# Kernel tuning notes

Measured on AMD Instinct MI355X. Metric: run time of the kernel, lower is better.

The kernel has to match this reference:

```python
import jax, jax.numpy as jnp
import numpy as np

DIM = 1024
N_HEADS = 16
HEAD_DIM = DIM // N_HEADS
HIDDEN = 2816
SEQ = 4096
BATCH = 1
NORM_EPS = 1e-5


def setup_inputs() -> dict:
    key = jax.random.key(0)
    ks = jax.random.split(key, 9)
    s = 1.0 / np.sqrt(DIM)
    return {
        "x": jax.random.normal(ks[0], (BATCH, SEQ, DIM), jnp.float32),
        "wq": jax.random.normal(ks[1], (DIM, DIM), jnp.float32) * s,
        "wk": jax.random.normal(ks[2], (DIM, DIM), jnp.float32) * s,
        "wv": jax.random.normal(ks[3], (DIM, DIM), jnp.float32) * s,
        "wo": jax.random.normal(ks[4], (DIM, DIM), jnp.float32) * s,
        "w1": jax.random.normal(ks[5], (DIM, HIDDEN), jnp.float32) * s,
        "w2": jax.random.normal(ks[6], (HIDDEN, DIM), jnp.float32) / np.sqrt(HIDDEN),
        "w3": jax.random.normal(ks[7], (DIM, HIDDEN), jnp.float32) * s,
        "g_attn_norm": jnp.ones((DIM,), jnp.float32),
        "g_ffn_norm": jnp.ones((DIM,), jnp.float32),
    }


def rmsnorm(x, g):
    # x: [b, s, d]; compute in fp32 as in the torch module, then cast back
    xf = x.astype(jnp.float32)
    n = xf * jax.lax.rsqrt(jnp.mean(xf * xf, axis=-1, keepdims=True) + NORM_EPS)
    return n.astype(x.dtype) * g


def attention(x, wq, wk, wv, wo):
    b, s, _ = x.shape
    q = (x @ wq).reshape(b, s, N_HEADS, HEAD_DIM).transpose(0, 2, 1, 3)  # [b,h,s,hd]
    k = (x @ wk).reshape(b, s, N_HEADS, HEAD_DIM).transpose(0, 2, 1, 3)
    v = (x @ wv).reshape(b, s, N_HEADS, HEAD_DIM).transpose(0, 2, 1, 3)
    scores = jnp.einsum("bhqd,bhkd->bhqk", q, k) / np.sqrt(HEAD_DIM)
    causal = jnp.tril(jnp.ones((s, s), bool))
    scores = jnp.where(causal, scores, -jnp.inf)
    probs = jax.nn.softmax(scores.astype(jnp.float32), axis=-1).astype(q.dtype)
    out = jnp.einsum("bhqk,bhkd->bhqd", probs, v)
    out = out.transpose(0, 2, 1, 3).reshape(b, s, DIM)
    return out @ wo


def feed_forward(x, w1, w2, w3):
    return (jax.nn.silu(x @ w1) * (x @ w3)) @ w2


def reference(x, wq, wk, wv, wo, w1, w2, w3, g_attn_norm, g_ffn_norm):
    h = x + attention(rmsnorm(x, g_attn_norm), wq, wk, wv, wo)
    out = h + feed_forward(rmsnorm(h, g_ffn_norm), w1, w2, w3)
    return out
```

## Files before the change

kernel.cpp:

```cpp
#include <hip/hip_runtime.h>
#include <stdint.h>


typedef unsigned short u16;
typedef unsigned int u32;
typedef __attribute__((ext_vector_type(8))) short short8;
typedef __attribute__((ext_vector_type(4))) float f32x4;

#define GLD16(G, L) __builtin_amdgcn_global_load_lds( \
    (__attribute__((address_space(1))) void*)(G),      \
    (__attribute__((address_space(3))) void*)(L), 16, 0, 0)

__device__ __forceinline__ u16 f2bf(float f) {
  u32 u = __builtin_bit_cast(u32, f);
  u32 r = u + 0x7fffu + ((u >> 16) & 1u);
  return (u16)(r >> 16);
}
__device__ __forceinline__ float bf2f(u16 b) {
  u32 u = (u32)b << 16;
  return __builtin_bit_cast(float, u);
}
__device__ __forceinline__ u32 pk_bf16(float lo, float hi) {
  u32 r;
  asm("v_cvt_pk_bf16_f32 %0, %1, %2" : "=v"(r) : "v"(lo), "v"(hi));
  return r;
}

__global__ __launch_bounds__(256) void k_tc4(const float* __restrict__ s0,
                                             const float* __restrict__ s1,
                                             const float* __restrict__ s2,
                                             const float* __restrict__ s3,
                                             u16* __restrict__ out, int R, int C) {
  const int z = blockIdx.z;
  const float* in = (z == 0) ? s0 : (z == 1) ? s1 : (z == 2) ? s2 : s3;
  u16* o = out + (size_t)z * R * C;
  __shared__ float t[32][33];
  const int tx = threadIdx.x & 31, ty = threadIdx.x >> 5;
  const int c0 = blockIdx.x * 32, r0 = blockIdx.y * 32;
#pragma unroll
  for (int i = 0; i < 32; i += 8)
    t[ty + i][tx] = in[(size_t)(r0 + ty + i) * C + (c0 + tx)];
  __syncthreads();
#pragma unroll
  for (int i = 0; i < 32; i += 8)
    o[(size_t)(c0 + ty + i) * R + (r0 + tx)] = f2bf(t[tx][ty + i]);
}

__global__ __launch_bounds__(256) void k_rms(const float* __restrict__ x,
                                             const float* __restrict__ g,
                                             u16* __restrict__ o) {
  const int row = blockIdx.x, tid = threadIdx.x;
  const float4 v = ((const float4*)(x + (size_t)row * 1024))[tid];
  float ss = v.x * v.x + v.y * v.y + v.z * v.z + v.w * v.w;
#pragma unroll
  for (int ofs = 32; ofs > 0; ofs >>= 1) ss += __shfl_xor(ss, ofs);
  __shared__ float red[4];
  if ((tid & 63) == 0) red[tid >> 6] = ss;
  __syncthreads();
  const float s = rsqrtf((red[0] + red[1] + red[2] + red[3]) * (1.f / 1024.f) + 1e-5f);
  const float4 gv = ((const float4*)g)[tid];
  u32 lo = (u32)f2bf(v.x * s * gv.x) | ((u32)f2bf(v.y * s * gv.y) << 16);
  u32 hi = (u32)f2bf(v.z * s * gv.z) | ((u32)f2bf(v.w * s * gv.w) << 16);
  *(uint2*)(o + (size_t)row * 1024 + tid * 4) = make_uint2(lo, hi);
}

template <int EPI, int TN>
__global__ __launch_bounds__(256) void k_gemm(const u16* __restrict__ A,
                                              const u16* __restrict__ Bt,
                                              u16* __restrict__ Obf,
                                              float* __restrict__ Of,
                                              const float* __restrict__ Rz,
                                              int M, int N, int K) {
  constexpr int NFR = TN / 32;
  __shared__ __align__(16) u16 As[2][128 * 32];
  __shared__ __align__(16) u16 Bs[2][TN * 32];
  const int tid = threadIdx.x;
  const int lane = tid & 63, wave = tid >> 6;
  const int wr = wave >> 1, wc = wave & 1;
  const int li = lane & 15, lg = lane >> 4;
  const int row0 = blockIdx.y * 128, col0 = blockIdx.x * TN;

  f32x4 acc[4][NFR] = {};
  const int sr = tid >> 2, sc = (tid & 3) * 8;
  const u16* ag = A + (size_t)(row0 + sr) * K + sc;
  const u16* bg = Bt + (size_t)(col0 + sr) * K + sc;
  const size_t rstep = (size_t)64 * K;

  GLD16(ag, &As[0][tid * 8]);
  GLD16(ag + rstep, &As[0][tid * 8 + 2048]);
  GLD16(bg, &Bs[0][tid * 8]);
  if constexpr (TN == 128) GLD16(bg + rstep, &Bs[0][tid * 8 + 2048]);
  __syncthreads();

  int cur = 0;
  for (int k0 = 0; k0 < K; k0 += 32) {
    const int nxt = cur ^ 1;
    if (k0 + 32 < K) {
      GLD16(ag + k0 + 32, &As[nxt][tid * 8]);
      GLD16(ag + rstep + k0 + 32, &As[nxt][tid * 8 + 2048]);
      GLD16(bg + k0 + 32, &Bs[nxt][tid * 8]);
      if constexpr (TN == 128) GLD16(bg + rstep + k0 + 32, &Bs[nxt][tid * 8 + 2048]);
    }
    short8 af[4], bfr[NFR];
#pragma unroll
    for (int m = 0; m < 4; ++m)
      af[m] = *(const short8*)(&As[cur][(wr * 64 + m * 16 + li) * 32 + lg * 8]);
#pragma unroll
    for (int n = 0; n < NFR; ++n)
      bfr[n] = *(const short8*)(&Bs[cur][(wc * (TN / 2) + n * 16 + li) * 32 + lg * 8]);
#pragma unroll
    for (int m = 0; m < 4; ++m)
#pragma unroll
      for (int n = 0; n < NFR; ++n)
        acc[m][n] = __builtin_amdgcn_mfma_f32_16x16x32_bf16(af[m], bfr[n], acc[m][n], 0, 0, 0);
    __syncthreads();
    cur = nxt;
  }

#pragma unroll
  for (int m = 0; m < 4; ++m) {
    const int row = row0 + wr * 64 + m * 16 + lg * 4;
#pragma unroll
    for (int n = 0; n < NFR; ++n) {
      const int col = col0 + wc * (TN / 2) + n * 16 + li;
#pragma unroll
      for (int r = 0; r < 4; ++r) {
        const size_t idx = (size_t)(row + r) * N + col;
        if (EPI == 0) Obf[idx] = f2bf(acc[m][n][r]);
        else          Of[idx] = acc[m][n][r] + Rz[idx];
      }
    }
  }
}

__global__ __launch_bounds__(256) void k_ffn13(const u16* __restrict__ A,
                                               const u16* __restrict__ B1,
                                               const u16* __restrict__ B3,
                                               u16* __restrict__ O,
                                               int M, int N, int K) {
  __shared__ __align__(16) u16 As[2][128 * 32];
  __shared__ __align__(16) u16 B1s[2][64 * 32];
  __shared__ __align__(16) u16 B3s[2][64 * 32];
  const int tid = threadIdx.x;
  const int lane = tid & 63, wave = tid >> 6;
  const int wr = wave >> 1, wc = wave & 1;
  const int li = lane & 15, lg = lane >> 4;
  const int row0 = blockIdx.y * 128, col0 = blockIdx.x * 64;

  f32x4 a1[4][2] = {}, a3[4][2] = {};
  const int sr = tid >> 2, sc = (tid & 3) * 8;
  const u16* ag = A + (size_t)(row0 + sr) * K + sc;
  const u16* b1g = B1 + (size_t)(col0 + sr) * K + sc;
  const u16* b3g = B3 + (size_t)(col0 + sr) * K + sc;
  const size_t rstep = (size_t)64 * K;

  GLD16(ag, &As[0][tid * 8]);
  GLD16(ag + rstep, &As[0][tid * 8 + 2048]);
  GLD16(b1g, &B1s[0][tid * 8]);
  GLD16(b3g, &B3s[0][tid * 8]);
  __syncthreads();

  int cur = 0;
  for (int k0 = 0; k0 < K; k0 += 32) {
    const int nxt = cur ^ 1;
    if (k0 + 32 < K) {
      GLD16(ag + k0 + 32, &As[nxt][tid * 8]);
      GLD16(ag + rstep + k0 + 32, &As[nxt][tid * 8 + 2048]);
      GLD16(b1g + k0 + 32, &B1s[nxt][tid * 8]);
      GLD16(b3g + k0 + 32, &B3s[nxt][tid * 8]);
    }
    short8 af[4], b1f[2], b3f[2];
#pragma unroll
    for (int m = 0; m < 4; ++m)
      af[m] = *(const short8*)(&As[cur][(wr * 64 + m * 16 + li) * 32 + lg * 8]);
#pragma unroll
    for (int n = 0; n < 2; ++n) {
      b1f[n] = *(const short8*)(&B1s[cur][(wc * 32 + n * 16 + li) * 32 + lg * 8]);
      b3f[n] = *(const short8*)(&B3s[cur][(wc * 32 + n * 16 + li) * 32 + lg * 8]);
    }
#pragma unroll
    for (int m = 0; m < 4; ++m)
#pragma unroll
      for (int n = 0; n < 2; ++n) {
        a1[m][n] = __builtin_amdgcn_mfma_f32_16x16x32_bf16(af[m], b1f[n], a1[m][n], 0, 0, 0);
        a3[m][n] = __builtin_amdgcn_mfma_f32_16x16x32_bf16(af[m], b3f[n], a3[m][n], 0, 0, 0);
      }
    __syncthreads();
    cur = nxt;
  }

#pragma unroll
  for (int m = 0; m < 4; ++m) {
    const int row = row0 + wr * 64 + m * 16 + lg * 4;
#pragma unroll
    for (int n = 0; n < 2; ++n) {
      const int col = col0 + wc * 32 + n * 16 + li;
#pragma unroll
      for (int r = 0; r < 4; ++r) {
        const float g1 = a1[m][n][r], g3 = a3[m][n][r];
        const float sl = g1 / (1.f + __expf(-g1));
        O[(size_t)(row + r) * N + col] = f2bf(sl * g3);
      }
    }
  }
}

__global__ __launch_bounds__(512) void k_attn(const u16* __restrict__ qkv,
                                              u16* __restrict__ Opart,
                                              float* __restrict__ ml) {
  const int LD = 3072;
  const int b = blockIdx.x;
  const int h = b & 15;
  const int p = (b >> 4) >> 1;
  const int j = (b >> 4) & 1;
  const int tid = threadIdx.x, lane = tid & 63, w = tid >> 6;
  const int li = lane & 15, lg = lane >> 4;
  const int swzB = (li & 7) << 4;
  const float QS = 0.125f * 1.44269504f;
  const float FM = 12.0f;

  __shared__ __align__(16) u16 Ks[64 * 64];
  __shared__ __align__(16) u16 Vt[64 * 64];
  __shared__ __align__(16) u16 Ps[8 * 16 * 64];

  const int krow = tid >> 3;
  const u16* kg = qkv + 1024 + h * 64 + ((tid & 7) ^ (krow & 7)) * 8;
  u16* klds = Ks + tid * 8;

  const int vd0 = (tid & 31) * 2;
  const int vkq = tid >> 5;
  const u16* vg = qkv + 2048 + h * 64 + vd0;
  u16* vl0 = Vt + (size_t)vd0 * 64 + (((vkq * 8) ^ ((vd0 & 7) << 4)) >> 1);
  u16* vl1 = Vt + (size_t)(vd0 + 1) * 64 + (((vkq * 8) ^ (((vd0 + 1) & 7) << 4)) >> 1);
  u16* pw = Ps + w * 1024 + li * 64;

  for (int sub = 0; sub < 2; ++sub) {
    const int qb = sub ? (31 - p) : p;
    const int q0 = qb * 128;
    const int t0 = j ? (qb + 1) : 0;
    const int t1 = j ? (2 * qb + 2) : (qb + 1);
    const int qrow = q0 + w * 16 + li;
    const int wqmax = q0 + w * 16 + 15;

    const u16* qp = qkv + (size_t)qrow * LD + h * 64;
    short8 qf0, qf1;
#pragma unroll
    for (int jj = 0; jj < 8; ++jj) {
      qf0[jj] = (short)f2bf(bf2f(qp[lg * 8 + jj]) * QS);
      qf1[jj] = (short)f2bf(bf2f(qp[32 + lg * 8 + jj]) * QS);
    }

    float lsm = 0.f;
    f32x4 accO[4] = {};
    uint4 kld;
    u32 vld[4];
    kld = *(const uint4*)(kg + (size_t)(t0 * 64 + krow) * LD);
#pragma unroll
    for (int i = 0; i < 4; ++i)
      vld[i] = *(const u32*)(vg + (size_t)(t0 * 64 + vkq * 4 + i) * LD);

    for (int t = t0; t < t1; ++t) {
      const int k0 = t * 64;
      __syncthreads();
      *(uint4*)klds = kld;
      {
        u32 lo0 = (vld[0] & 0xffffu) | (vld[1] << 16);
        u32 lo1 = (vld[2] & 0xffffu) | (vld[3] << 16);
        u32 hi0 = (vld[0] >> 16) | (vld[1] & 0xffff0000u);
        u32 hi1 = (vld[2] >> 16) | (vld[3] & 0xffff0000u);
        *(uint2*)vl0 = make_uint2(lo0, lo1);
        *(uint2*)vl1 = make_uint2(hi0, hi1);
      }
      __syncthreads();
      if (t + 1 < t1) {
        kld = *(const uint4*)(kg + (size_t)((t + 1) * 64 + krow) * LD);
        const u16* vp = vg + (size_t)(t + 1) * 64 * LD;
#pragma unroll
        for (int i = 0; i < 4; ++i) vld[i] = *(const u32*)(vp + (size_t)(vkq * 4 + i) * LD);
      }

      if (k0 <= wqmax) {
        f32x4 st[4];
#pragma unroll
        for (int f = 0; f < 4; ++f) {
          const u16* kp = Ks + (size_t)(f * 16 + li) * 64;
          const short8 ka0 = *(const short8*)(kp + (((lg * 16) ^ swzB) >> 1));
          const short8 ka1 = *(const short8*)(kp + (((64 + lg * 16) ^ swzB) >> 1));
          f32x4 z = {-FM, -FM, -FM, -FM};
          z = __builtin_amdgcn_mfma_f32_16x16x32_bf16(ka0, qf0, z, 0, 0, 0);
          st[f] = __builtin_amdgcn_mfma_f32_16x16x32_bf16(ka1, qf1, z, 0, 0, 0);
        }
        if (!(k0 + 63 <= q0 + w * 16)) {
#pragma unroll
          for (int f = 0; f < 4; ++f)
#pragma unroll
            for (int r = 0; r < 4; ++r) {
              const int kg2 = k0 + f * 16 + lg * 4 + r;
              if (kg2 > qrow) st[f][r] = -1e30f;
            }
        }
        float psum = 0.f;
#pragma unroll
        for (int f = 0; f < 4; ++f) {
          const float p0 = __builtin_amdgcn_exp2f(st[f][0]);
          const float p1 = __builtin_amdgcn_exp2f(st[f][1]);
          const float p2 = __builtin_amdgcn_exp2f(st[f][2]);
          const float p3 = __builtin_amdgcn_exp2f(st[f][3]);
          psum += (p0 + p1) + (p2 + p3);
          *(uint2*)(pw + (((f * 32 + lg * 8) ^ swzB) >> 1)) =
              make_uint2(pk_bf16(p0, p1), pk_bf16(p2, p3));
        }
        psum += __shfl_xor(psum, 16);
        psum += __shfl_xor(psum, 32);
        lsm += psum;

#pragma unroll
        for (int kk = 0; kk < 2; ++kk) {
          const int cofs = ((kk * 64 + lg * 16) ^ swzB) >> 1;
          const short8 pf = *(const short8*)(pw + cofs);
#pragma unroll
          for (int n = 0; n < 4; ++n) {
            const short8 vf = *(const short8*)(Vt + (size_t)(n * 16 + li) * 64 + cofs);
            accO[n] = __builtin_amdgcn_mfma_f32_16x16x32_bf16(vf, pf, accO[n], 0, 0, 0);
          }
        }
      }
    }

    const int item = (h * 32 + qb) * 2 + j;
    u16* op = Opart + (size_t)item * 8192 + (w * 16 + li) * 64 + lg * 4;
#pragma unroll
    for (int n = 0; n < 4; ++n)
      *(uint2*)(op + n * 16) = make_uint2(pk_bf16(accO[n][0], accO[n][1]),
                                          pk_bf16(accO[n][2], accO[n][3]));
    if (lg == 0) ml[item * 128 + w * 16 + li] = lsm;
  }
}

__global__ __launch_bounds__(256) void k_amerge(const u16* __restrict__ Opart,
                                                const float* __restrict__ ml,
                                                u16* __restrict__ o) {
  const int b = blockIdx.x;
  const int h = b & 15, qb = b >> 4;
  const int q = threadIdx.x >> 1;
  const int dh = (threadIdx.x & 1) * 32;
  const int i0 = (h * 32 + qb) * 2;
  const float l0 = ml[i0 * 128 + q];
  const float l1 = ml[(i0 + 1) * 128 + q];
  const float r = 1.f / (l0 + l1);
  const u16* p0 = Opart + (size_t)i0 * 8192 + q * 64 + dh;
  const u16* p1 = p0 + 8192;
  u16* op = o + (size_t)(qb * 128 + q) * 1024 + h * 64 + dh;
#pragma unroll
  for (int dd = 0; dd < 32; dd += 4) {
    const uint2 a = *(const uint2*)(p0 + dd);
    const uint2 c = *(const uint2*)(p1 + dd);
    const float s0 = bf2f((u16)a.x) + bf2f((u16)c.x);
    const float s1 = bf2f((u16)(a.x >> 16)) + bf2f((u16)(c.x >> 16));
    const float s2 = bf2f((u16)a.y) + bf2f((u16)c.y);
    const float s3 = bf2f((u16)(a.y >> 16)) + bf2f((u16)(c.y >> 16));
    *(uint2*)(op + dd) = make_uint2(pk_bf16(s0 * r, s1 * r), pk_bf16(s2 * r, s3 * r));
  }
}

extern "C" void kernel_launch(void* const* d_in, const int* in_sizes, int n_in,
                              void* d_out, int out_size, void* d_ws, size_t ws_size,
                              hipStream_t stream) {
  const float* x  = (const float*)d_in[0];
  const float* wq = (const float*)d_in[1];
  const float* wk = (const float*)d_in[2];
  const float* wv = (const float*)d_in[3];
  const float* wo = (const float*)d_in[4];
  const float* w1 = (const float*)d_in[5];
  const float* w2 = (const float*)d_in[6];
  const float* w3 = (const float*)d_in[7];
  const float* ga = (const float*)d_in[8];
  const float* gf = (const float*)d_in[9];
  float* out = (float*)d_out;

  char* p = (char*)d_ws;
  auto take = [&](size_t n) { char* r = p; p += (n + 255) & ~(size_t)255; return r; };
  u16* wqkvo_t = (u16*)take(4ull * 1024 * 1024 * 2);
  u16* w13_t   = (u16*)take(2ull * 2816 * 1024 * 2);
  u16* w2_t    = (u16*)take(1024ull * 2816 * 2);
  u16* xn      = (u16*)take(4096ull * 1024 * 2);
  u16* qkvb    = (u16*)take(4096ull * 3072 * 2);
  u16* atn     = (u16*)take(4096ull * 1024 * 2);
  char* uni    = take(48234496);
  u16* Opart   = (u16*)uni;
  float* mlb   = (float*)(uni + 1024ull * 8192 * 2);
  float* hb    = (float*)uni;
  u16* hn      = (u16*)(uni + 4096ull * 1024 * 4);
  u16* ffb     = (u16*)(uni + 4096ull * 1024 * 6);

  u16* wqkv_t = wqkvo_t;
  u16* wo_t   = wqkvo_t + 3ull * 1024 * 1024;
  u16* w1_t   = w13_t;
  u16* w3_t   = w13_t + 2816ull * 1024;

  k_tc4<<<dim3(32, 32, 4), 256, 0, stream>>>(wq, wk, wv, wo, wqkvo_t, 1024, 1024);
  k_tc4<<<dim3(88, 32, 2), 256, 0, stream>>>(w1, w3, w1, w3, w13_t, 1024, 2816);
  k_tc4<<<dim3(32, 88, 1), 256, 0, stream>>>(w2, w2, w2, w2, w2_t, 2816, 1024);

  k_rms<<<4096, 256, 0, stream>>>(x, ga, xn);
  k_gemm<0, 128><<<dim3(24, 32), 256, 0, stream>>>(xn, wqkv_t, qkvb, nullptr, nullptr, 4096, 3072, 1024);
  k_attn<<<512, 512, 0, stream>>>(qkvb, Opart, mlb);
  k_amerge<<<512, 256, 0, stream>>>(Opart, mlb, atn);
  k_gemm<1, 64><<<dim3(16, 32), 256, 0, stream>>>(atn, wo_t, nullptr, hb, x, 4096, 1024, 1024);
  k_rms<<<4096, 256, 0, stream>>>(hb, gf, hn);
  k_ffn13<<<dim3(44, 32), 256, 0, stream>>>(hn, w1_t, w3_t, ffb, 4096, 2816, 1024);
  k_gemm<1, 64><<<dim3(16, 32), 256, 0, stream>>>(ffb, w2_t, nullptr, out, hb, 4096, 1024, 2816);
}
```

Baseline: 262.3 us.

## Merge weight transpose launches and split attention into one work item per block

The three weight-transpose launches are folded into a single kernel that picks its matrix from a flat block index, which saves two launch overheads. The attention kernel stops pairing a short and a long query block inside one workgroup. It now launches 1024 blocks, each handling one (head, query block, key half) item, with the heaviest query blocks ordered first so the hardware scheduler can balance load dynamically. The cost is more blocks with uneven work, plus repeated per-block setup such as Q fragment loads and pointer math.

```diff
diff --git a/kernel.cpp b/kernel.cpp
--- a/kernel.cpp
+++ b/kernel.cpp
@@ -26,17 +26,41 @@
   return r;
 }
 
-__global__ __launch_bounds__(256) void k_tc4(const float* __restrict__ s0,
-                                             const float* __restrict__ s1,
-                                             const float* __restrict__ s2,
-                                             const float* __restrict__ s3,
-                                             u16* __restrict__ out, int R, int C) {
-  const int z = blockIdx.z;
-  const float* in = (z == 0) ? s0 : (z == 1) ? s1 : (z == 2) ? s2 : s3;
-  u16* o = out + (size_t)z * R * C;
+__global__ __launch_bounds__(256) void k_prep(const float* __restrict__ wq,
+                                              const float* __restrict__ wk,
+                                              const float* __restrict__ wv,
+                                              const float* __restrict__ wo,
+                                              const float* __restrict__ w1,
+                                              const float* __restrict__ w3,
+                                              const float* __restrict__ w2f,
+                                              u16* __restrict__ wqkvo_t,
+                                              u16* __restrict__ w13_t,
+                                              u16* __restrict__ w2_t) {
+  const int bid = blockIdx.x;
+  const float* in;
+  u16* o;
+  int R, C, c0, r0;
+  if (bid < 4096) {
+    const int z = bid >> 10, r = bid & 1023;
+    in = (z == 0) ? wq : (z == 1) ? wk : (z == 2) ? wv : wo;
+    o = wqkvo_t + (size_t)z * 1024 * 1024;
+    R = 1024; C = 1024;
+    c0 = (r & 31) * 32; r0 = (r >> 5) * 32;
+  } else if (bid < 9728) {
+    int r = bid - 4096;
+    const int z = r / 2816; r %= 2816;
+    in = z ? w3 : w1;
+    o = w13_t + (size_t)z * 2816 * 1024;
+    R = 1024; C = 2816;
+    c0 = (r % 88) * 32; r0 = (r / 88) * 32;
+  } else {
+    const int r = bid - 9728;
+    in = w2f; o = w2_t;
+    R = 2816; C = 1024;
+    c0 = (r & 31) * 32; r0 = (r >> 5) * 32;
+  }
   __shared__ float t[32][33];
   const int tx = threadIdx.x & 31, ty = threadIdx.x >> 5;
-  const int c0 = blockIdx.x * 32, r0 = blockIdx.y * 32;
 #pragma unroll
   for (int i = 0; i < 32; i += 8)
     t[ty + i][tx] = in[(size_t)(r0 + ty + i) * C + (c0 + tx)];
@@ -209,10 +233,10 @@
                                               u16* __restrict__ Opart,
                                               float* __restrict__ ml) {
   const int LD = 3072;
-  const int b = blockIdx.x;
-  const int h = b & 15;
-  const int p = (b >> 4) >> 1;
-  const int j = (b >> 4) & 1;
+  const int bid = blockIdx.x;
+  const int qb = 31 - (bid >> 5);
+  const int h = (bid >> 1) & 15;
+  const int j = bid & 1;
   const int tid = threadIdx.x, lane = tid & 63, w = tid >> 6;
   const int li = lane & 15, lg = lane >> 4;
   const int swzB = (li & 7) << 4;
@@ -234,107 +258,104 @@
   u16* vl1 = Vt + (size_t)(vd0 + 1) * 64 + (((vkq * 8) ^ (((vd0 + 1) & 7) << 4)) >> 1);
   u16* pw = Ps + w * 1024 + li * 64;
 
-  for (int sub = 0; sub < 2; ++sub) {
-    const int qb = sub ? (31 - p) : p;
-    const int q0 = qb * 128;
-    const int t0 = j ? (qb + 1) : 0;
-    const int t1 = j ? (2 * qb + 2) : (qb + 1);
-    const int qrow = q0 + w * 16 + li;
-    const int wqmax = q0 + w * 16 + 15;
-
-    const u16* qp = qkv + (size_t)qrow * LD + h * 64;
-    short8 qf0, qf1;
-#pragma unroll
-    for (int jj = 0; jj < 8; ++jj) {
-      qf0[jj] = (short)f2bf(bf2f(qp[lg * 8 + jj]) * QS);
-      qf1[jj] = (short)f2bf(bf2f(qp[32 + lg * 8 + jj]) * QS);
-    }
-
-    float lsm = 0.f;
-    f32x4 accO[4] = {};
-    uint4 kld;
-    u32 vld[4];
-    kld = *(const uint4*)(kg + (size_t)(t0 * 64 + krow) * LD);
-#pragma unroll
-    for (int i = 0; i < 4; ++i)
-      vld[i] = *(const u32*)(vg + (size_t)(t0 * 64 + vkq * 4 + i) * LD);
-
-    for (int t = t0; t < t1; ++t) {
-      const int k0 = t * 64;
-      __syncthreads();
-      *(uint4*)klds = kld;
-      {
-        u32 lo0 = (vld[0] & 0xffffu) | (vld[1] << 16);
-        u32 lo1 = (vld[2] & 0xffffu) | (vld[3] << 16);
-        u32 hi0 = (vld[0] >> 16) | (vld[1] & 0xffff0000u);
-        u32 hi1 = (vld[2] >> 16) | (vld[3] & 0xffff0000u);
-        *(uint2*)vl0 = make_uint2(lo0, lo1);
-        *(uint2*)vl1 = make_uint2(hi0, hi1);
-      }
-      __syncthreads();
-      if (t + 1 < t1) {
-        kld = *(const uint4*)(kg + (size_t)((t + 1) * 64 + krow) * LD);
-        const u16* vp = vg + (size_t)(t + 1) * 64 * LD;
-#pragma unroll
-        for (int i = 0; i < 4; ++i) vld[i] = *(const u32*)(vp + (size_t)(vkq * 4 + i) * LD);
-      }
-
-      if (k0 <= wqmax) {
-        f32x4 st[4];
-#pragma unroll
-        for (int f = 0; f < 4; ++f) {
-          const u16* kp = Ks + (size_t)(f * 16 + li) * 64;
-          const short8 ka0 = *(const short8*)(kp + (((lg * 16) ^ swzB) >> 1));
-          const short8 ka1 = *(const short8*)(kp + (((64 + lg * 16) ^ swzB) >> 1));
-          f32x4 z = {-FM, -FM, -FM, -FM};
-          z = __builtin_amdgcn_mfma_f32_16x16x32_bf16(ka0, qf0, z, 0, 0, 0);
-          st[f] = __builtin_amdgcn_mfma_f32_16x16x32_bf16(ka1, qf1, z, 0, 0, 0);
+  const int q0 = qb * 128;
+  const int t0 = j ? (qb + 1) : 0;
+  const int t1 = j ? (2 * qb + 2) : (qb + 1);
+  const int qrow = q0 + w * 16 + li;
+  const int wqmax = q0 + w * 16 + 15;
+
+  const u16* qp = qkv + (size_t)qrow * LD + h * 64;
+  short8 qf0, qf1;
+#pragma unroll
+  for (int jj = 0; jj < 8; ++jj) {
+    qf0[jj] = (short)f2bf(bf2f(qp[lg * 8 + jj]) * QS);
+    qf1[jj] = (short)f2bf(bf2f(qp[32 + lg * 8 + jj]) * QS);
+  }
+
+  float lsm = 0.f;
+  f32x4 accO[4] = {};
+  uint4 kld;
+  u32 vld[4];
+  kld = *(const uint4*)(kg + (size_t)(t0 * 64 + krow) * LD);
+#pragma unroll
+  for (int i = 0; i < 4; ++i)
+    vld[i] = *(const u32*)(vg + (size_t)(t0 * 64 + vkq * 4 + i) * LD);
+
+  for (int t = t0; t < t1; ++t) {
+    const int k0 = t * 64;
+    __syncthreads();
+    *(uint4*)klds = kld;
+    {
+      u32 lo0 = (vld[0] & 0xffffu) | (vld[1] << 16);
+      u32 lo1 = (vld[2] & 0xffffu) | (vld[3] << 16);
+      u32 hi0 = (vld[0] >> 16) | (vld[1] & 0xffff0000u);
+      u32 hi1 = (vld[2] >> 16) | (vld[3] & 0xffff0000u);
+      *(uint2*)vl0 = make_uint2(lo0, lo1);
+      *(uint2*)vl1 = make_uint2(hi0, hi1);
+    }
+    __syncthreads();
+    if (t + 1 < t1) {
+      kld = *(const uint4*)(kg + (size_t)((t + 1) * 64 + krow) * LD);
+      const u16* vp = vg + (size_t)(t + 1) * 64 * LD;
+#pragma unroll
+      for (int i = 0; i < 4; ++i) vld[i] = *(const u32*)(vp + (size_t)(vkq * 4 + i) * LD);
+    }
+
+    if (k0 <= wqmax) {
+      f32x4 st[4];
+#pragma unroll
+      for (int f = 0; f < 4; ++f) {
+        const u16* kp = Ks + (size_t)(f * 16 + li) * 64;
+        const short8 ka0 = *(const short8*)(kp + (((lg * 16) ^ swzB) >> 1));
+        const short8 ka1 = *(const short8*)(kp + (((64 + lg * 16) ^ swzB) >> 1));
+        f32x4 z = {-FM, -FM, -FM, -FM};
+        z = __builtin_amdgcn_mfma_f32_16x16x32_bf16(ka0, qf0, z, 0, 0, 0);
+        st[f] = __builtin_amdgcn_mfma_f32_16x16x32_bf16(ka1, qf1, z, 0, 0, 0);
+      }
+      if (!(k0 + 63 <= q0 + w * 16)) {
+#pragma unroll
+        for (int f = 0; f < 4; ++f)
+#pragma unroll
+          for (int r = 0; r < 4; ++r) {
+            const int kg2 = k0 + f * 16 + lg * 4 + r;
+            if (kg2 > qrow) st[f][r] = -1e30f;
+          }
+      }
+      float psum = 0.f;
+#pragma unroll
+      for (int f = 0; f < 4; ++f) {
+        const float p0 = __builtin_amdgcn_exp2f(st[f][0]);
+        const float p1 = __builtin_amdgcn_exp2f(st[f][1]);
+        const float p2 = __builtin_amdgcn_exp2f(st[f][2]);
+        const float p3 = __builtin_amdgcn_exp2f(st[f][3]);
+        psum += (p0 + p1) + (p2 + p3);
+        *(uint2*)(pw + (((f * 32 + lg * 8) ^ swzB) >> 1)) =
+            make_uint2(pk_bf16(p0, p1), pk_bf16(p2, p3));
+      }
+      psum += __shfl_xor(psum, 16);
+      psum += __shfl_xor(psum, 32);
+      lsm += psum;
+
+#pragma unroll
+      for (int kk = 0; kk < 2; ++kk) {
+        const int cofs = ((kk * 64 + lg * 16) ^ swzB) >> 1;
+        const short8 pf = *(const short8*)(pw + cofs);
+#pragma unroll
+        for (int n = 0; n < 4; ++n) {
+          const short8 vf = *(const short8*)(Vt + (size_t)(n * 16 + li) * 64 + cofs);
+          accO[n] = __builtin_amdgcn_mfma_f32_16x16x32_bf16(vf, pf, accO[n], 0, 0, 0);
         }
-        if (!(k0 + 63 <= q0 + w * 16)) {
-#pragma unroll
-          for (int f = 0; f < 4; ++f)
-#pragma unroll
-            for (int r = 0; r < 4; ++r) {
-              const int kg2 = k0 + f * 16 + lg * 4 + r;
-              if (kg2 > qrow) st[f][r] = -1e30f;
-            }
-        }
-        float psum = 0.f;
-#pragma unroll
-        for (int f = 0; f < 4; ++f) {
-          const float p0 = __builtin_amdgcn_exp2f(st[f][0]);
-          const float p1 = __builtin_amdgcn_exp2f(st[f][1]);
-          const float p2 = __builtin_amdgcn_exp2f(st[f][2]);
-          const float p3 = __builtin_amdgcn_exp2f(st[f][3]);
-          psum += (p0 + p1) + (p2 + p3);
-          *(uint2*)(pw + (((f * 32 + lg * 8) ^ swzB) >> 1)) =
-              make_uint2(pk_bf16(p0, p1), pk_bf16(p2, p3));
-        }
-        psum += __shfl_xor(psum, 16);
-        psum += __shfl_xor(psum, 32);
-        lsm += psum;
-
-#pragma unroll
-        for (int kk = 0; kk < 2; ++kk) {
-          const int cofs = ((kk * 64 + lg * 16) ^ swzB) >> 1;
-          const short8 pf = *(const short8*)(pw + cofs);
-#pragma unroll
-          for (int n = 0; n < 4; ++n) {
-            const short8 vf = *(const short8*)(Vt + (size_t)(n * 16 + li) * 64 + cofs);
-            accO[n] = __builtin_amdgcn_mfma_f32_16x16x32_bf16(vf, pf, accO[n], 0, 0, 0);
-          }
-        }
-      }
-    }
-
-    const int item = (h * 32 + qb) * 2 + j;
-    u16* op = Opart + (size_t)item * 8192 + (w * 16 + li) * 64 + lg * 4;
-#pragma unroll
-    for (int n = 0; n < 4; ++n)
-      *(uint2*)(op + n * 16) = make_uint2(pk_bf16(accO[n][0], accO[n][1]),
-                                          pk_bf16(accO[n][2], accO[n][3]));
-    if (lg == 0) ml[item * 128 + w * 16 + li] = lsm;
-  }
+      }
+    }
+  }
+
+  const int item = (h * 32 + qb) * 2 + j;
+  u16* op = Opart + (size_t)item * 8192 + (w * 16 + li) * 64 + lg * 4;
+#pragma unroll
+  for (int n = 0; n < 4; ++n)
+    *(uint2*)(op + n * 16) = make_uint2(pk_bf16(accO[n][0], accO[n][1]),
+                                        pk_bf16(accO[n][2], accO[n][3]));
+  if (lg == 0) ml[item * 128 + w * 16 + li] = lsm;
 }
 
 __global__ __launch_bounds__(256) void k_amerge(const u16* __restrict__ Opart,
@@ -398,13 +419,11 @@
   u16* w1_t   = w13_t;
   u16* w3_t   = w13_t + 2816ull * 1024;
 
-  k_tc4<<<dim3(32, 32, 4), 256, 0, stream>>>(wq, wk, wv, wo, wqkvo_t, 1024, 1024);
-  k_tc4<<<dim3(88, 32, 2), 256, 0, stream>>>(w1, w3, w1, w3, w13_t, 1024, 2816);
-  k_tc4<<<dim3(32, 88, 1), 256, 0, stream>>>(w2, w2, w2, w2, w2_t, 2816, 1024);
+  k_prep<<<12544, 256, 0, stream>>>(wq, wk, wv, wo, w1, w3, w2, wqkvo_t, w13_t, w2_t);
 
   k_rms<<<4096, 256, 0, stream>>>(x, ga, xn);
   k_gemm<0, 128><<<dim3(24, 32), 256, 0, stream>>>(xn, wqkv_t, qkvb, nullptr, nullptr, 4096, 3072, 1024);
-  k_attn<<<512, 512, 0, stream>>>(qkvb, Opart, mlb);
+  k_attn<<<1024, 512, 0, stream>>>(qkvb, Opart, mlb);
   k_amerge<<<512, 256, 0, stream>>>(Opart, mlb, atn);
   k_gemm<1, 64><<<dim3(16, 32), 256, 0, stream>>>(atn, wo_t, nullptr, hb, x, 4096, 1024, 1024);
   k_rms<<<4096, 256, 0, stream>>>(hb, gf, hn);
```

Result: no change. 260.3 us (-0.7%).
